# Performance work log

Hardware: AMD Instinct MI355X
Metric: run time of the kernel (lower is better)

The kernel has to match this reference:

```python
import jax, jax.numpy as jnp
import numpy as np

N_NODES = 50000
N_EDGES = 800000
D_IN = 64
D_HID = 64
N_LAYERS = 3


def setup_inputs() -> dict:
    key = jax.random.key(0)
    ks = jax.random.split(key, 3 + 2 * N_LAYERS)
    x = jax.random.normal(ks[0], (N_NODES, D_IN), dtype=jnp.float32)
    edge_index = jax.random.randint(ks[1], (2, N_EDGES), 0, N_NODES, dtype=jnp.int64)
    edge_weight = jax.random.uniform(ks[2], (N_EDGES,), dtype=jnp.float32)
    inp = {"x": x, "edge_index": edge_index, "edge_weight": edge_weight}
    dims = [(D_IN, D_HID)] + [(D_HID, D_HID)] * (N_LAYERS - 1)
    for i, (din, dout) in enumerate(dims):
        # Glorot-style init like PyG GCNConv
        scale = jnp.sqrt(6.0 / (din + dout)).astype(jnp.float32)
        inp[f"W{i}"] = jax.random.uniform(ks[3 + 2 * i], (din, dout), dtype=jnp.float32, minval=-1.0, maxval=1.0) * scale
        inp[f"b{i}"] = jnp.zeros((dout,), dtype=jnp.float32)
    return inp


def _gcn_norm(edge_index, edge_weight, num_nodes, dtype):
    # Add self-loops with weight 1, then symmetric normalization (PyG gcn_norm).
    loop = jnp.arange(num_nodes)
    src = jnp.concatenate([edge_index[0], loop])
    dst = jnp.concatenate([edge_index[1], loop])
    w = jnp.concatenate([edge_weight, jnp.ones((num_nodes,), dtype=dtype)])
    deg = jax.ops.segment_sum(w, dst, num_segments=num_nodes)  # [N]
    dinv = jnp.where(deg > 0, jax.lax.rsqrt(deg), jnp.zeros_like(deg))
    norm = dinv[src] * w * dinv[dst]  # [E+N]
    return src, dst, norm


def reference(x, edge_index, edge_weight, W0, b0, W1, b1, W2, b2):
    N = x.shape[0]
    src, dst, norm = _gcn_norm(edge_index, edge_weight, N, x.dtype)
    for W, b in ((W0, b0), (W1, b1), (W2, b2)):
        h = x @ W                                   # [N, dout] linear first (PyG)
        msg = h[src] * norm[:, None]                # gather + scale per edge
        x = jax.ops.segment_sum(msg, dst, num_segments=N) + b  # scatter-add + bias
        x = jax.nn.relu(x)
    return x
```

## Files before the change

kernel.cpp:

```cpp
#include <hip/hip_runtime.h>

#define NN 50000
#define NE 800000
#define NB 782
#define NBLK 256
#define CHUNK 3125
#define CAP 1536
#define CAPTOT (NB * CAP)

typedef float f32x4 __attribute__((ext_vector_type(4)));

__device__ __forceinline__ float blo(unsigned u) { return __uint_as_float(u << 16); }
__device__ __forceinline__ float bhi(unsigned u) { return __uint_as_float(u & 0xFFFF0000u); }
__device__ __forceinline__ unsigned short f2b(float f) {
    unsigned u = __float_as_uint(f);
    return (unsigned short)((u + 0x7FFFu + ((u >> 16) & 1u)) >> 16);
}

__global__ __launch_bounds__(256) void p12(const int* __restrict__ src,
        const int* __restrict__ dst, const float* __restrict__ w,
        int* __restrict__ cursor, int2* __restrict__ stage) {
    __shared__ unsigned se[CHUNK];
    __shared__ float    sw[CHUNK];
    __shared__ int      lh[NB];
    int t = threadIdx.x;
    for (int i = t; i < NB; i += 256) lh[i] = 0;
    __syncthreads();
    int e0 = blockIdx.x * CHUNK;
    for (int i = t; i < CHUNK; i += 256) {
        int e = e0 + i;
        unsigned d = (unsigned)dst[e];
        unsigned s = (unsigned)src[e];
        float wv = w[e];
        unsigned pk = 0xFFFFFFFFu;
        if (d < NN) {
            pk = (s & 0xFFFFu) | ((d & 63u) << 16) | ((d >> 6) << 22);
            atomicAdd(&lh[d >> 6], 1);
        }
        se[i] = pk;
        sw[i] = wv;
    }
    __syncthreads();
    for (int i = t; i < NB; i += 256) {
        int c = lh[i];
        lh[i] = c ? (i * CAP + atomicAdd(&cursor[i], c)) : 0;
    }
    __syncthreads();
    for (int i = t; i < CHUNK; i += 256) {
        unsigned pk = se[i];
        if (pk != 0xFFFFFFFFu) {
            int bucket = (int)(pk >> 22);
            int pos = atomicAdd(&lh[bucket], 1);
            if (pos < (bucket + 1) * CAP)
                stage[pos] = make_int2((int)(pk & 0x3FFFFFu), __float_as_int(sw[i]));
        }
    }
}

__global__ __launch_bounds__(256) void p3_sort(const int2* __restrict__ stage,
        const int* __restrict__ cursor, unsigned* __restrict__ csr4,
        int* __restrict__ row_ptr, int* __restrict__ row_deg, float* __restrict__ dinv) {
    __shared__ int   hist[64];
    __shared__ int   cur[64];
    __shared__ float wsum[64];
    int b = blockIdx.x, t = threadIdx.x;
    int g0 = b * CAP;
    int cnt = cursor[b];
    if (cnt > CAP) cnt = CAP;
    int g1 = g0 + cnt;
    if (t < 64) { hist[t] = 0; wsum[t] = 0.f; }
    __syncthreads();
    for (int j = g0 + t; j < g1; j += 256) {
        int2 pk = stage[j];
        int r = (pk.x >> 16) & 63;
        atomicAdd(&hist[r], 1);
        atomicAdd(&wsum[r], __int_as_float(pk.y));
    }
    __syncthreads();
    if (t == 0) {
        int s = g0;
        for (int r = 0; r < 64; ++r) { cur[r] = s; s += hist[r]; }
    }
    __syncthreads();
    if (t < 64) {
        int n = b * 64 + t;
        if (n < NN) {
            row_ptr[n] = cur[t];
            row_deg[n] = hist[t];
            dinv[n] = rsqrtf(wsum[t] + 1.0f);
        }
    }
    __syncthreads();
    for (int j = g0 + t; j < g1; j += 256) {
        int2 pk = stage[j];
        int r = (pk.x >> 16) & 63;
        int pos = atomicAdd(&cur[r], 1);
        csr4[pos] = (unsigned)(pk.x & 0xFFFF) |
                    ((unsigned)f2b(__int_as_float(pk.y)) << 16);
    }
}

__global__ __launch_bounds__(256) void gemm_pre_kernel(const float* __restrict__ x,
        const float* __restrict__ W, const float* __restrict__ dinv,
        unsigned short* __restrict__ hp) {
    __shared__ float xs[16][64];
    int t = threadIdx.x;
    int base = blockIdx.x * 16;
    for (int idx = t; idx < 16 * 64; idx += 256)
        xs[idx >> 6][idx & 63] = x[(size_t)(base + (idx >> 6)) * 64 + (idx & 63)];
    __syncthreads();
    int col = t & 63, rq = t >> 6;
    float wc[64];
#pragma unroll
    for (int k = 0; k < 64; ++k) wc[k] = W[k * 64 + col];
    float a0 = 0.f, a1 = 0.f, a2 = 0.f, a3 = 0.f;
#pragma unroll
    for (int k = 0; k < 64; ++k) {
        float wk = wc[k];
        a0 += xs[rq     ][k] * wk;
        a1 += xs[rq +  4][k] * wk;
        a2 += xs[rq +  8][k] * wk;
        a3 += xs[rq + 12][k] * wk;
    }
    int r = base + rq;
    hp[(size_t)(r     ) * 64 + col] = f2b(dinv[r     ] * a0);
    hp[(size_t)(r +  4) * 64 + col] = f2b(dinv[r +  4] * a1);
    hp[(size_t)(r +  8) * 64 + col] = f2b(dinv[r +  8] * a2);
    hp[(size_t)(r + 12) * 64 + col] = f2b(dinv[r + 12] * a3);
}

__device__ __forceinline__ float4 gather_row(int n, int fq, int qbase,
        const int* __restrict__ row_ptr, const int* __restrict__ row_deg,
        const unsigned* __restrict__ csr4, const uint2* __restrict__ hp64) {
    int s0 = row_ptr[n];
    int s1 = s0 + row_deg[n];
    uint2 self = hp64[(size_t)n * 16 + fq];
    float ax = blo(self.x), ay = bhi(self.x), az = blo(self.y), aw = bhi(self.y);
    float bx = 0.f, by = 0.f, bz = 0.f, bw = 0.f;
    for (int base = s0; base < s1; base += 16) {
        int j = base + fq;
        unsigned meta = 0u;
        if (j < s1) meta = __builtin_nontemporal_load(&csr4[j]);
        int m = s1 - base; if (m > 16) m = 16;
        int jj = 0;
        for (; jj + 4 <= m; jj += 4) {
            unsigned m0 = __shfl(meta, qbase + jj + 0);
            unsigned m1 = __shfl(meta, qbase + jj + 1);
            unsigned m2 = __shfl(meta, qbase + jj + 2);
            unsigned m3 = __shfl(meta, qbase + jj + 3);
            uint2 u0 = hp64[(size_t)(m0 & 0xFFFFu) * 16 + fq];
            uint2 u1 = hp64[(size_t)(m1 & 0xFFFFu) * 16 + fq];
            uint2 u2 = hp64[(size_t)(m2 & 0xFFFFu) * 16 + fq];
            uint2 u3 = hp64[(size_t)(m3 & 0xFFFFu) * 16 + fq];
            float w0 = __uint_as_float(m0 & 0xFFFF0000u);
            float w1 = __uint_as_float(m1 & 0xFFFF0000u);
            float w2 = __uint_as_float(m2 & 0xFFFF0000u);
            float w3 = __uint_as_float(m3 & 0xFFFF0000u);
            ax += w0 * blo(u0.x); ay += w0 * bhi(u0.x); az += w0 * blo(u0.y); aw += w0 * bhi(u0.y);
            bx += w1 * blo(u1.x); by += w1 * bhi(u1.x); bz += w1 * blo(u1.y); bw += w1 * bhi(u1.y);
            ax += w2 * blo(u2.x); ay += w2 * bhi(u2.x); az += w2 * blo(u2.y); aw += w2 * bhi(u2.y);
            bx += w3 * blo(u3.x); by += w3 * bhi(u3.x); bz += w3 * blo(u3.y); bw += w3 * bhi(u3.y);
        }
        for (; jj < m; ++jj) {
            unsigned mm = __shfl(meta, qbase + jj);
            uint2 u0 = hp64[(size_t)(mm & 0xFFFFu) * 16 + fq];
            float w0 = __uint_as_float(mm & 0xFFFF0000u);
            ax += w0 * blo(u0.x); ay += w0 * bhi(u0.x); az += w0 * blo(u0.y); aw += w0 * bhi(u0.y);
        }
    }
    return make_float4(ax + bx, ay + by, az + bz, aw + bw);
}

__global__ __launch_bounds__(256) void fused_kernel(const int* __restrict__ row_ptr,
        const int* __restrict__ row_deg, const unsigned* __restrict__ csr4,
        const float* __restrict__ dinv, const uint2* __restrict__ hp_cur,
        const float* __restrict__ bias, const float* __restrict__ Wn,
        unsigned short* __restrict__ hp_next) {
    __shared__ float ys[16][64];
    int t = threadIdx.x;
    int lane = t & 63, q = lane >> 4, fq = lane & 15;
    int ni = ((t >> 6) << 2) + q;
    int n = blockIdx.x * 16 + ni;
    float4 g = gather_row(n, fq, q << 4, row_ptr, row_deg, csr4, hp_cur);
    float dv = dinv[n];
    float4 bb = ((const float4*)bias)[fq];
    float4 y;
    y.x = fmaxf(dv * g.x + bb.x, 0.f);
    y.y = fmaxf(dv * g.y + bb.y, 0.f);
    y.z = fmaxf(dv * g.z + bb.z, 0.f);
    y.w = fmaxf(dv * g.w + bb.w, 0.f);
    ((float4*)ys[ni])[fq] = y;
    __syncthreads();
    int col = lane, rq = t >> 6;
    float wc[64];
#pragma unroll
    for (int k = 0; k < 64; ++k) wc[k] = Wn[k * 64 + col];
    float a0 = 0.f, a1 = 0.f, a2 = 0.f, a3 = 0.f;
#pragma unroll
    for (int k = 0; k < 64; ++k) {
        float wk = wc[k];
        a0 += ys[rq     ][k] * wk;
        a1 += ys[rq +  4][k] * wk;
        a2 += ys[rq +  8][k] * wk;
        a3 += ys[rq + 12][k] * wk;
    }
    int r = blockIdx.x * 16 + rq;
    __builtin_nontemporal_store(f2b(dinv[r     ] * a0), &hp_next[(size_t)(r     ) * 64 + col]);
    __builtin_nontemporal_store(f2b(dinv[r +  4] * a1), &hp_next[(size_t)(r +  4) * 64 + col]);
    __builtin_nontemporal_store(f2b(dinv[r +  8] * a2), &hp_next[(size_t)(r +  8) * 64 + col]);
    __builtin_nontemporal_store(f2b(dinv[r + 12] * a3), &hp_next[(size_t)(r + 12) * 64 + col]);
}

__global__ __launch_bounds__(256) void final_kernel(const int* __restrict__ row_ptr,
        const int* __restrict__ row_deg, const unsigned* __restrict__ csr4,
        const float* __restrict__ dinv, const uint2* __restrict__ hp_cur,
        const float* __restrict__ bias, float* __restrict__ out) {
    int t = threadIdx.x;
    int lane = t & 63, q = lane >> 4, fq = lane & 15;
    int n = blockIdx.x * 16 + ((t >> 6) << 2) + q;
    float4 g = gather_row(n, fq, q << 4, row_ptr, row_deg, csr4, hp_cur);
    float dv = dinv[n];
    float4 bb = ((const float4*)bias)[fq];
    f32x4 r;
    r.x = fmaxf(dv * g.x + bb.x, 0.f);
    r.y = fmaxf(dv * g.y + bb.y, 0.f);
    r.z = fmaxf(dv * g.z + bb.z, 0.f);
    r.w = fmaxf(dv * g.w + bb.w, 0.f);
    __builtin_nontemporal_store(r, &((f32x4*)out)[(size_t)n * 16 + fq]);
}

extern "C" void kernel_launch(void* const* d_in, const int* in_sizes, int n_in,
                              void* d_out, int out_size, void* d_ws, size_t ws_size,
                              hipStream_t stream) {
    const float* x  = (const float*)d_in[0];
    const int*   ei = (const int*)d_in[1];
    const float* ew = (const float*)d_in[2];
    const float* W0 = (const float*)d_in[3];
    const float* b0 = (const float*)d_in[4];
    const float* W1 = (const float*)d_in[5];
    const float* b1 = (const float*)d_in[6];
    const float* W2 = (const float*)d_in[7];
    const float* b2 = (const float*)d_in[8];
    float*       out = (float*)d_out;

    const int* src = ei;
    const int* dst = ei + NE;

    int2*     stage   = (int2*)d_ws;
    unsigned* csr4    = (unsigned*)(stage + CAPTOT);
    int*      cursor  = (int*)(csr4 + CAPTOT);
    int*      row_ptr = cursor + NB;
    int*      row_deg = row_ptr + NN;
    float*    dinv    = (float*)(row_deg + NN);
    unsigned short* hpA = (unsigned short*)(dinv + NN);
    unsigned short* hpB = hpA + (size_t)NN * 64;

    (void)hipMemsetAsync(cursor, 0, NB * sizeof(int), stream);
    p12<<<NBLK, 256, 0, stream>>>(src, dst, ew, cursor, stage);
    p3_sort<<<NB, 256, 0, stream>>>(stage, cursor, csr4, row_ptr, row_deg, dinv);

    gemm_pre_kernel<<<NN / 16, 256, 0, stream>>>(x, W0, dinv, hpA);
    fused_kernel<<<NN / 16, 256, 0, stream>>>(row_ptr, row_deg, csr4, dinv,
            (const uint2*)hpA, b0, W1, hpB);
    fused_kernel<<<NN / 16, 256, 0, stream>>>(row_ptr, row_deg, csr4, dinv,
            (const uint2*)hpB, b1, W2, hpA);
    final_kernel<<<NN / 16, 256, 0, stream>>>(row_ptr, row_deg, csr4, dinv,
            (const uint2*)hpA, b2, out);
}
```

Before: 203.9 us.

## Permute nodes by in-degree within 64-node buckets to balance gather waves

In the sort pass, nodes inside each 64-node bucket are ranked by degree and given permuted positions, so the sixteen-node groups processed together have similar edge counts and less wavefront divergence. Row metadata is packed into one int2, and a new remap kernel rewrites CSR source indices into the permuted space. The first GEMM gathers x rows through the permutation and the final kernel scatters output back to original order. This adds a full pass over the CSR array, an extra launch and indirect loads. It also drops the nontemporal stores in the fused kernel.

```diff
diff --git a/kernel.cpp b/kernel.cpp
--- a/kernel.cpp
+++ b/kernel.cpp
@@ -59,9 +59,12 @@
 
 __global__ __launch_bounds__(256) void p3_sort(const int2* __restrict__ stage,
         const int* __restrict__ cursor, unsigned* __restrict__ csr4,
-        int* __restrict__ row_ptr, int* __restrict__ row_deg, float* __restrict__ dinv) {
+        int2* __restrict__ rowinfo, float* __restrict__ dinv,
+        int* __restrict__ p2o, int* __restrict__ inv) {
     __shared__ int   hist[64];
+    __shared__ int   start[64];
     __shared__ int   cur[64];
+    __shared__ int   key[64];
     __shared__ float wsum[64];
     int b = blockIdx.x, t = threadIdx.x;
     int g0 = b * CAP;
@@ -79,15 +82,27 @@
     __syncthreads();
     if (t == 0) {
         int s = g0;
-        for (int r = 0; r < 64; ++r) { cur[r] = s; s += hist[r]; }
+        for (int r = 0; r < 64; ++r) { start[r] = s; s += hist[r]; }
+    }
+    __syncthreads();
+    if (t < 64) {
+        cur[t] = start[t];
+        key[t] = (b * 64 + t < NN) ? hist[t] : 0x7FFFFFFF;
     }
     __syncthreads();
     if (t < 64) {
         int n = b * 64 + t;
         if (n < NN) {
-            row_ptr[n] = cur[t];
-            row_deg[n] = hist[t];
-            dinv[n] = rsqrtf(wsum[t] + 1.0f);
+            int kt = key[t], rank = 0;
+            for (int j = 0; j < 64; ++j) {
+                int kj = key[j];
+                rank += (kj < kt) || (kj == kt && j < t);
+            }
+            int p = b * 64 + rank;
+            rowinfo[p] = make_int2(start[t], hist[t]);
+            dinv[p] = rsqrtf(wsum[t] + 1.0f);
+            p2o[p] = n;
+            inv[n] = p;
         }
     }
     __syncthreads();
@@ -100,41 +115,54 @@
     }
 }
 
-__global__ __launch_bounds__(256) void gemm_pre_kernel(const float* __restrict__ x,
+__global__ __launch_bounds__(256) void remap_kernel(unsigned* __restrict__ csr4,
+                                                    const int* __restrict__ inv) {
+    int j = blockIdx.x * 256 + threadIdx.x;
+    if (j < CAPTOT) {
+        unsigned v = csr4[j];
+        unsigned s = v & 0xFFFFu;
+        if (s < NN) csr4[j] = (v & 0xFFFF0000u) | (unsigned)inv[s];
+    }
+}
+
+__global__ __launch_bounds__(256) void gemm0_kernel(const float* __restrict__ x,
         const float* __restrict__ W, const float* __restrict__ dinv,
-        unsigned short* __restrict__ hp) {
+        const int* __restrict__ p2o, unsigned short* __restrict__ hp) {
     __shared__ float xs[16][64];
     int t = threadIdx.x;
     int base = blockIdx.x * 16;
-    for (int idx = t; idx < 16 * 64; idx += 256)
-        xs[idx >> 6][idx & 63] = x[(size_t)(base + (idx >> 6)) * 64 + (idx & 63)];
-    __syncthreads();
-    int col = t & 63, rq = t >> 6;
+    int grp = t >> 6, l = t & 63;
+    for (int rr = grp; rr < 16; rr += 4) {
+        int orig = p2o[base + rr];
+        xs[rr][l] = x[(size_t)orig * 64 + l];
+    }
+    __syncthreads();
     float wc[64];
 #pragma unroll
-    for (int k = 0; k < 64; ++k) wc[k] = W[k * 64 + col];
+    for (int k = 0; k < 64; ++k) wc[k] = W[k * 64 + l];
     float a0 = 0.f, a1 = 0.f, a2 = 0.f, a3 = 0.f;
 #pragma unroll
     for (int k = 0; k < 64; ++k) {
         float wk = wc[k];
-        a0 += xs[rq     ][k] * wk;
-        a1 += xs[rq +  4][k] * wk;
-        a2 += xs[rq +  8][k] * wk;
-        a3 += xs[rq + 12][k] * wk;
-    }
-    int r = base + rq;
-    hp[(size_t)(r     ) * 64 + col] = f2b(dinv[r     ] * a0);
-    hp[(size_t)(r +  4) * 64 + col] = f2b(dinv[r +  4] * a1);
-    hp[(size_t)(r +  8) * 64 + col] = f2b(dinv[r +  8] * a2);
-    hp[(size_t)(r + 12) * 64 + col] = f2b(dinv[r + 12] * a3);
-}
-
-__device__ __forceinline__ float4 gather_row(int n, int fq, int qbase,
-        const int* __restrict__ row_ptr, const int* __restrict__ row_deg,
-        const unsigned* __restrict__ csr4, const uint2* __restrict__ hp64) {
-    int s0 = row_ptr[n];
-    int s1 = s0 + row_deg[n];
-    uint2 self = hp64[(size_t)n * 16 + fq];
+        a0 += xs[grp     ][k] * wk;
+        a1 += xs[grp +  4][k] * wk;
+        a2 += xs[grp +  8][k] * wk;
+        a3 += xs[grp + 12][k] * wk;
+    }
+    int r = base + grp;
+    hp[(size_t)(r     ) * 64 + l] = f2b(dinv[r     ] * a0);
+    hp[(size_t)(r +  4) * 64 + l] = f2b(dinv[r +  4] * a1);
+    hp[(size_t)(r +  8) * 64 + l] = f2b(dinv[r +  8] * a2);
+    hp[(size_t)(r + 12) * 64 + l] = f2b(dinv[r + 12] * a3);
+}
+
+__device__ __forceinline__ float4 gather_row(int p, int fq, int qbase,
+        const int2* __restrict__ rowinfo, const unsigned* __restrict__ csr4,
+        const uint2* __restrict__ hp64) {
+    int2 ri = rowinfo[p];
+    int s0 = ri.x;
+    int s1 = ri.x + ri.y;
+    uint2 self = hp64[(size_t)p * 16 + fq];
     float ax = blo(self.x), ay = bhi(self.x), az = blo(self.y), aw = bhi(self.y);
     float bx = 0.f, by = 0.f, bz = 0.f, bw = 0.f;
     for (int base = s0; base < s1; base += 16) {
@@ -171,17 +199,16 @@
     return make_float4(ax + bx, ay + by, az + bz, aw + bw);
 }
 
-__global__ __launch_bounds__(256) void fused_kernel(const int* __restrict__ row_ptr,
-        const int* __restrict__ row_deg, const unsigned* __restrict__ csr4,
-        const float* __restrict__ dinv, const uint2* __restrict__ hp_cur,
-        const float* __restrict__ bias, const float* __restrict__ Wn,
-        unsigned short* __restrict__ hp_next) {
+__global__ __launch_bounds__(256) void fused_kernel(const int2* __restrict__ rowinfo,
+        const unsigned* __restrict__ csr4, const float* __restrict__ dinv,
+        const uint2* __restrict__ hp_cur, const float* __restrict__ bias,
+        const float* __restrict__ Wn, unsigned short* __restrict__ hp_next) {
     __shared__ float ys[16][64];
     int t = threadIdx.x;
     int lane = t & 63, q = lane >> 4, fq = lane & 15;
     int ni = ((t >> 6) << 2) + q;
     int n = blockIdx.x * 16 + ni;
-    float4 g = gather_row(n, fq, q << 4, row_ptr, row_deg, csr4, hp_cur);
+    float4 g = gather_row(n, fq, q << 4, rowinfo, csr4, hp_cur);
     float dv = dinv[n];
     float4 bb = ((const float4*)bias)[fq];
     float4 y;
@@ -205,20 +232,20 @@
         a3 += ys[rq + 12][k] * wk;
     }
     int r = blockIdx.x * 16 + rq;
-    __builtin_nontemporal_store(f2b(dinv[r     ] * a0), &hp_next[(size_t)(r     ) * 64 + col]);
-    __builtin_nontemporal_store(f2b(dinv[r +  4] * a1), &hp_next[(size_t)(r +  4) * 64 + col]);
-    __builtin_nontemporal_store(f2b(dinv[r +  8] * a2), &hp_next[(size_t)(r +  8) * 64 + col]);
-    __builtin_nontemporal_store(f2b(dinv[r + 12] * a3), &hp_next[(size_t)(r + 12) * 64 + col]);
-}
-
-__global__ __launch_bounds__(256) void final_kernel(const int* __restrict__ row_ptr,
-        const int* __restrict__ row_deg, const unsigned* __restrict__ csr4,
-        const float* __restrict__ dinv, const uint2* __restrict__ hp_cur,
-        const float* __restrict__ bias, float* __restrict__ out) {
+    hp_next[(size_t)(r     ) * 64 + col] = f2b(dinv[r     ] * a0);
+    hp_next[(size_t)(r +  4) * 64 + col] = f2b(dinv[r +  4] * a1);
+    hp_next[(size_t)(r +  8) * 64 + col] = f2b(dinv[r +  8] * a2);
+    hp_next[(size_t)(r + 12) * 64 + col] = f2b(dinv[r + 12] * a3);
+}
+
+__global__ __launch_bounds__(256) void final_kernel(const int2* __restrict__ rowinfo,
+        const unsigned* __restrict__ csr4, const float* __restrict__ dinv,
+        const uint2* __restrict__ hp_cur, const float* __restrict__ bias,
+        const int* __restrict__ p2o, float* __restrict__ out) {
     int t = threadIdx.x;
     int lane = t & 63, q = lane >> 4, fq = lane & 15;
     int n = blockIdx.x * 16 + ((t >> 6) << 2) + q;
-    float4 g = gather_row(n, fq, q << 4, row_ptr, row_deg, csr4, hp_cur);
+    float4 g = gather_row(n, fq, q << 4, rowinfo, csr4, hp_cur);
     float dv = dinv[n];
     float4 bb = ((const float4*)bias)[fq];
     f32x4 r;
@@ -226,7 +253,8 @@
     r.y = fmaxf(dv * g.y + bb.y, 0.f);
     r.z = fmaxf(dv * g.z + bb.z, 0.f);
     r.w = fmaxf(dv * g.w + bb.w, 0.f);
-    __builtin_nontemporal_store(r, &((f32x4*)out)[(size_t)n * 16 + fq]);
+    int orig = p2o[n];
+    __builtin_nontemporal_store(r, &((f32x4*)out)[(size_t)orig * 16 + fq]);
 }
 
 extern "C" void kernel_launch(void* const* d_in, const int* in_sizes, int n_in,
@@ -247,23 +275,25 @@
     const int* dst = ei + NE;
 
     int2*     stage   = (int2*)d_ws;
-    unsigned* csr4    = (unsigned*)(stage + CAPTOT);
+    int2*     rowinfo = stage + CAPTOT;
+    unsigned* csr4    = (unsigned*)(rowinfo + NN);
     int*      cursor  = (int*)(csr4 + CAPTOT);
-    int*      row_ptr = cursor + NB;
-    int*      row_deg = row_ptr + NN;
-    float*    dinv    = (float*)(row_deg + NN);
-    unsigned short* hpA = (unsigned short*)(dinv + NN);
+    float*    dinv    = (float*)(cursor + NB);
+    int*      p2o     = (int*)(dinv + NN);
+    int*      inv     = p2o + NN;
+    unsigned short* hpA = (unsigned short*)(inv + NN);
     unsigned short* hpB = hpA + (size_t)NN * 64;
 
     (void)hipMemsetAsync(cursor, 0, NB * sizeof(int), stream);
     p12<<<NBLK, 256, 0, stream>>>(src, dst, ew, cursor, stage);
-    p3_sort<<<NB, 256, 0, stream>>>(stage, cursor, csr4, row_ptr, row_deg, dinv);
-
-    gemm_pre_kernel<<<NN / 16, 256, 0, stream>>>(x, W0, dinv, hpA);
-    fused_kernel<<<NN / 16, 256, 0, stream>>>(row_ptr, row_deg, csr4, dinv,
+    p3_sort<<<NB, 256, 0, stream>>>(stage, cursor, csr4, rowinfo, dinv, p2o, inv);
+    remap_kernel<<<(CAPTOT + 255) / 256, 256, 0, stream>>>(csr4, inv);
+
+    gemm0_kernel<<<NN / 16, 256, 0, stream>>>(x, W0, dinv, p2o, hpA);
+    fused_kernel<<<NN / 16, 256, 0, stream>>>(rowinfo, csr4, dinv,
             (const uint2*)hpA, b0, W1, hpB);
-    fused_kernel<<<NN / 16, 256, 0, stream>>>(row_ptr, row_deg, csr4, dinv,
+    fused_kernel<<<NN / 16, 256, 0, stream>>>(rowinfo, csr4, dinv,
             (const uint2*)hpB, b1, W2, hpA);
-    final_kernel<<<NN / 16, 256, 0, stream>>>(row_ptr, row_deg, csr4, dinv,
-            (const uint2*)hpA, b2, out);
-}
+    final_kernel<<<NN / 16, 256, 0, stream>>>(rowinfo, csr4, dinv,
+            (const uint2*)hpA, b2, p2o, out);
+}
```

After: 213.3 us. 1.05x slower.
